# Kernel optimization log

Hardware: AMD Instinct MI355X
Metric: run time of the kernel (lower is better)

Reference implementation:

```python
import jax, jax.numpy as jnp
import numpy as np


def _mish(x):
    # mish(x) = x * tanh(softplus(x))
    return x * jnp.tanh(jax.nn.softplus(x))


def setup_inputs() -> dict:
    key = jax.random.key(0)
    k1, k2, k3 = jax.random.split(key, 3)
    x = jax.random.normal(k1, (128, 3, 256, 256), dtype=jnp.float32)
    weight = jax.random.normal(k2, (16, 3, 3, 3), dtype=jnp.float32) * 0.1
    bias = jax.random.normal(k3, (16,), dtype=jnp.float32) * 0.1
    return {"x": x, "weight": weight, "bias": bias}


def reference(x, weight, bias):
    # Valid conv2d (stride 1, no padding), NCHW / OIHW layout
    y = jax.lax.conv_general_dilated(
        x, weight,
        window_strides=(1, 1),
        padding='VALID',
        dimension_numbers=('NCHW', 'OIHW', 'NCHW'))
    y = y + bias[None, :, None, None]
    # two Mish activations
    return _mish(_mish(y))
```

## Files before the change

kernel.cpp:

```cpp
#include <hip/hip_runtime.h>

#define N_  128
#define IC_ 3
#define OC_ 16
#define H_  256
#define W_  256
#define OH_ 254
#define OW_ 254

__device__ __forceinline__ float mish_f(float x) {
    float e = __expf(x);
    float p = 1.0f + e;
    float t = p * p;
    float r = x * (t - 1.0f) * __builtin_amdgcn_rcpf(t + 1.0f);
    return (x > 20.0f) ? x : r;
}

__global__ __launch_bounds__(256) void conv_mish_kernel(
    const float* __restrict__ x, const float* __restrict__ w,
    const float* __restrict__ bias, float* __restrict__ out)
{
    __shared__ float sw[27 * 16];
    __shared__ float sb[16];
    int t = threadIdx.x;
    for (int i = t; i < 432; i += 256) {
        int oc = i / 27;
        int r  = i - oc * 27;
        sw[r * 16 + oc] = w[i];
    }
    if (t < 16) sb[t] = bias[t];
    __syncthreads();

    int p    = t & 127;
    int row2 = t >> 7;
    int oh   = blockIdx.x * 2 + row2;
    int n    = blockIdx.y;
    if (p >= 127) return;
    int ow0  = p * 2;

    float acc0[16], acc1[16];
    #pragma unroll
    for (int oc = 0; oc < 16; ++oc) { float b = sb[oc]; acc0[oc] = b; acc1[oc] = b; }

    const float* xb = x + (size_t)n * (IC_ * H_ * W_);

    #pragma unroll 1
    for (int s = 0; s < 9; ++s) {
        int ic = s / 3;
        int kh = s - ic * 3;
        const float* rowp = xb + ic * (H_ * W_) + (oh + kh) * W_ + ow0;
        float2 a  = *(const float2*)(rowp);
        float2 b2 = *(const float2*)(rowp + 2);
        float in0 = a.x, in1 = a.y, in2 = b2.x, in3 = b2.y;
        const float4* wbase = (const float4*)(&sw[s * 48]);
        #pragma unroll
        for (int kw = 0; kw < 3; ++kw) {
            float i0 = (kw == 0) ? in0 : (kw == 1) ? in1 : in2;
            float i1 = (kw == 0) ? in1 : (kw == 1) ? in2 : in3;
            #pragma unroll
            for (int q = 0; q < 4; ++q) {
                float4 wv = wbase[kw * 4 + q];
                acc0[q*4+0] += wv.x * i0;  acc1[q*4+0] += wv.x * i1;
                acc0[q*4+1] += wv.y * i0;  acc1[q*4+1] += wv.y * i1;
                acc0[q*4+2] += wv.z * i0;  acc1[q*4+2] += wv.z * i1;
                acc0[q*4+3] += wv.w * i0;  acc1[q*4+3] += wv.w * i1;
            }
        }
    }

    float* ob = out + (size_t)n * (OC_ * OH_ * OW_) + (size_t)oh * OW_ + ow0;
    #pragma unroll
    for (int oc = 0; oc < 16; ++oc) {
        float v0 = mish_f(mish_f(acc0[oc]));
        float v1 = mish_f(mish_f(acc1[oc]));
        *(float2*)(ob + (size_t)oc * (OH_ * OW_)) = make_float2(v0, v1);
    }
}

extern "C" void kernel_launch(void* const* d_in, const int* in_sizes, int n_in,
                              void* d_out, int out_size, void* d_ws, size_t ws_size,
                              hipStream_t stream) {
    const float* x = (const float*)d_in[0];
    const float* w = (const float*)d_in[1];
    const float* b = (const float*)d_in[2];
    float* o = (float*)d_out;
    dim3 grid(OH_ / 2, N_);
    dim3 block(256);
    conv_mish_kernel<<<grid, block, 0, stream>>>(x, w, b, o);
}
```

Baseline: 680.4 us.

## Pack conv math into float2 ops, prepack weights, use nontemporal stores

Moves the weight transposition into a separate tiny kernel writing to workspace, so the main kernel reads weights and bias straight from global memory with no shared memory or barrier. Accumulation and the Mish math use 2-wide float vectors so the compiler can emit packed FMA and multiply instructions. The overflow check becomes a clamp on t. Output stores are nontemporal to avoid polluting cache. The cost is an extra kernel launch, plus weight loads that now go through scalar/global memory instead of LDS.

```diff
diff --git a/kernel.cpp b/kernel.cpp
--- a/kernel.cpp
+++ b/kernel.cpp
@@ -8,29 +8,39 @@
 #define OH_ 254
 #define OW_ 254
 
-__device__ __forceinline__ float mish_f(float x) {
-    float e = __expf(x);
-    float p = 1.0f + e;
-    float t = p * p;
-    float r = x * (t - 1.0f) * __builtin_amdgcn_rcpf(t + 1.0f);
-    return (x > 20.0f) ? x : r;
+typedef float v2f __attribute__((ext_vector_type(2)));
+
+__device__ __forceinline__ v2f mish2(v2f x) {
+    v2f xe = x * 1.44269504088896340f;
+    v2f e;
+    e.x = __builtin_amdgcn_exp2f(xe.x);
+    e.y = __builtin_amdgcn_exp2f(xe.y);
+    v2f p = e + 1.0f;
+    v2f t = p * p;
+    v2f clampv = {1e30f, 1e30f};
+    t = __builtin_elementwise_min(t, clampv);
+    v2f num = (t - 1.0f) * x;
+    v2f den = t + 1.0f;
+    v2f r;
+    r.x = __builtin_amdgcn_rcpf(den.x);
+    r.y = __builtin_amdgcn_rcpf(den.y);
+    return num * r;
+}
+
+__global__ void repack_w(const float* __restrict__ w, float* __restrict__ pw) {
+    int i = threadIdx.x;
+    if (i < 432) {
+        int oc = i / 27;
+        int r  = i - oc * 27;
+        pw[r * 16 + oc] = w[i];
+    }
 }
 
 __global__ __launch_bounds__(256) void conv_mish_kernel(
-    const float* __restrict__ x, const float* __restrict__ w,
+    const float* __restrict__ x, const float* __restrict__ pw,
     const float* __restrict__ bias, float* __restrict__ out)
 {
-    __shared__ float sw[27 * 16];
-    __shared__ float sb[16];
-    int t = threadIdx.x;
-    for (int i = t; i < 432; i += 256) {
-        int oc = i / 27;
-        int r  = i - oc * 27;
-        sw[r * 16 + oc] = w[i];
-    }
-    if (t < 16) sb[t] = bias[t];
-    __syncthreads();
-
+    int t    = threadIdx.x;
     int p    = t & 127;
     int row2 = t >> 7;
     int oh   = blockIdx.x * 2 + row2;
@@ -38,11 +48,13 @@
     if (p >= 127) return;
     int ow0  = p * 2;
 
-    float acc0[16], acc1[16];
+    v2f acc0[8], acc1[8];
+    const v2f* bq = (const v2f*)bias;
     #pragma unroll
-    for (int oc = 0; oc < 16; ++oc) { float b = sb[oc]; acc0[oc] = b; acc1[oc] = b; }
+    for (int q = 0; q < 8; ++q) { v2f b = bq[q]; acc0[q] = b; acc1[q] = b; }
 
     const float* xb = x + (size_t)n * (IC_ * H_ * W_);
+    const v2f*   wv = (const v2f*)pw;
 
     #pragma unroll 1
     for (int s = 0; s < 9; ++s) {
@@ -51,29 +63,29 @@
         const float* rowp = xb + ic * (H_ * W_) + (oh + kh) * W_ + ow0;
         float2 a  = *(const float2*)(rowp);
         float2 b2 = *(const float2*)(rowp + 2);
-        float in0 = a.x, in1 = a.y, in2 = b2.x, in3 = b2.y;
-        const float4* wbase = (const float4*)(&sw[s * 48]);
+        float in[4] = {a.x, a.y, b2.x, b2.y};
         #pragma unroll
         for (int kw = 0; kw < 3; ++kw) {
-            float i0 = (kw == 0) ? in0 : (kw == 1) ? in1 : in2;
-            float i1 = (kw == 0) ? in1 : (kw == 1) ? in2 : in3;
+            v2f iv0 = {in[kw],     in[kw]};
+            v2f iv1 = {in[kw + 1], in[kw + 1]};
             #pragma unroll
-            for (int q = 0; q < 4; ++q) {
-                float4 wv = wbase[kw * 4 + q];
-                acc0[q*4+0] += wv.x * i0;  acc1[q*4+0] += wv.x * i1;
-                acc0[q*4+1] += wv.y * i0;  acc1[q*4+1] += wv.y * i1;
-                acc0[q*4+2] += wv.z * i0;  acc1[q*4+2] += wv.z * i1;
-                acc0[q*4+3] += wv.w * i0;  acc1[q*4+3] += wv.w * i1;
+            for (int q = 0; q < 8; ++q) {
+                v2f w2 = wv[s * 24 + kw * 8 + q];
+                acc0[q] += w2 * iv0;
+                acc1[q] += w2 * iv1;
             }
         }
     }
 
     float* ob = out + (size_t)n * (OC_ * OH_ * OW_) + (size_t)oh * OW_ + ow0;
     #pragma unroll
-    for (int oc = 0; oc < 16; ++oc) {
-        float v0 = mish_f(mish_f(acc0[oc]));
-        float v1 = mish_f(mish_f(acc1[oc]));
-        *(float2*)(ob + (size_t)oc * (OH_ * OW_)) = make_float2(v0, v1);
+    for (int q = 0; q < 8; ++q) {
+        v2f v0 = mish2(mish2(acc0[q]));
+        v2f v1 = mish2(mish2(acc1[q]));
+        v2f s0 = {v0.x, v1.x};
+        v2f s1 = {v0.y, v1.y};
+        __builtin_nontemporal_store(s0, (v2f*)(ob + (size_t)(2 * q)     * (OH_ * OW_)));
+        __builtin_nontemporal_store(s1, (v2f*)(ob + (size_t)(2 * q + 1) * (OH_ * OW_)));
     }
 }
 
@@ -83,8 +95,9 @@
     const float* x = (const float*)d_in[0];
     const float* w = (const float*)d_in[1];
     const float* b = (const float*)d_in[2];
-    float* o = (float*)d_out;
+    float* pw = (float*)d_ws;
+    repack_w<<<dim3(1), dim3(512), 0, stream>>>(w, pw);
     dim3 grid(OH_ / 2, N_);
     dim3 block(256);
-    conv_mish_kernel<<<grid, block, 0, stream>>>(x, w, b, o);
+    conv_mish_kernel<<<grid, block, 0, stream>>>(x, pw, b, (float*)d_out);
 }
```

New measurement: 604.3 us. -11.2%, faster.
